# Optimization experiments

Measured on AMD Instinct MI355X. Metric: run time of the kernel, lower is better.

Reference implementation:

```python
import jax, jax.numpy as jnp
import numpy as np
from jax import lax
from jax.scipy.linalg import solve_triangular

SR = 16000
FRAME_PERIOD = 80
FFT_LENGTH = 1024
WIN_MS = 30
EPS = 1e-05
DEFAULT_F0 = 150.0
B, T, N = 8, 320000, 4000

N_BAND = int(np.log2(SR / 600))  # 4
CUTOFF = [SR / 2 ** i for i in range(2, N_BAND + 1)]
CUTOFF.append(CUTOFF[-1])  # [4000, 2000, 1000, 1000]
SEG = [int(c * WIN_MS / 500 + 1.5) for c in CUTOFF]  # [241, 121, 61, 61]

_HHP_VALS = [0.00041447996898231424, 0.0007812505141729248, -0.0010917236836275842,
             -0.001986792567596759, 0.0020903896961562292, 0.004094057027284935,
             -0.0034025808529816698, -0.007496154127205602, 0.004972263339933064,
             0.012738791249119802, -0.006696032689574911, -0.020694051570247052,
             0.008432436565041345, 0.03307438375870053, -0.010018936738799522,
             -0.05423136140580825, 0.011293988915051487, 0.10020081367388213,
             -0.012120546202484579, -0.316300210390957, 0.5124068258062764]
_HLP_VALS = [-0.0006548817007748305, 7.561994958159384e-05, 0.0020408456937895227,
             -0.0007468053532203044, -0.004350223568826493, 0.0025966428382642732,
             0.007639602282756696, -0.006490411890149785, -0.011765804538954506,
             0.013649908479276255, 0.01636866479016021, -0.026075976030529347,
             -0.020910294856659444, 0.04826072503231665, 0.02476784661104811,
             -0.09617846758336064, -0.027359756709866623, 0.3148805216163004,
             0.5282734359405503]

def _qmf_high():
    h = np.zeros(41)
    h[:21] = _HHP_VALS
    h[21:] = h[19::-1]
    return h.astype(np.float32)

def _qmf_low():
    h = np.zeros(37)
    h[:19] = _HLP_VALS
    h[19:] = h[17::-1]
    return h.astype(np.float32)

def _make_window():
    w = np.zeros((N_BAND, SEG[0]), np.float32)
    for i, s in enumerate(SEG):
        w[i, :s] = np.hanning(s + 2)[1:-1]
    return w

def _interp_tables():
    coarse = np.concatenate([[0.0], [SR / 2 ** i for i in range(N_BAND, 0, -1)]])
    freq = np.arange(FFT_LENGTH // 2 + 1) * (SR / FFT_LENGTH)
    idx = np.clip(np.searchsorted(coarse, freq) - 1, 0, len(coarse) - 2)
    x0 = coarse[:-1]
    dx = coarse[1:] - x0
    wts = ((freq - x0[idx]) / dx[idx]).astype(np.float32)
    return idx.astype(np.int32), wts

_HHP = _qmf_high()
_HLP = _qmf_low()
_WIN = _make_window()
_IDX, _WTS = _interp_tables()


def _qmf_conv(x, h):
    # x: (B, T), h: (k,). Reflection pad k//2, cross-correlation, stride 2.
    p = h.shape[0] // 2
    xp = jnp.pad(x, ((0, 0), (p, p)), mode='reflect')
    out = lax.conv_general_dilated(xp[:, None, :], h[None, None, :], (2,), 'VALID',
                                   dimension_numbers=('NCH', 'OIH', 'NCH'))
    return out[:, 0, :]


def setup_inputs() -> dict:
    key = jax.random.key(0)
    k1, k2 = jax.random.split(key)
    x = jax.random.normal(k1, (B, T), jnp.float32)
    f0 = 100.0 + 200.0 * jax.random.uniform(k2, (B, N), jnp.float32)  # 100-300 Hz
    return {"x": x, "f0": f0}


def reference(x, f0):
    hHP = jnp.asarray(_HHP)
    hLP = jnp.asarray(_HLP)
    f0 = lax.stop_gradient(jnp.where(f0 <= 32, DEFAULT_F0, f0))
    Bn, Nf = f0.shape
    time_axis = jnp.arange(Nf, dtype=f0.dtype) * (FRAME_PERIOD / SR)
    bidx = jnp.arange(Bn)[:, None, None]
    eye6 = EPS * jnp.eye(6, dtype=x.dtype)
    lx = x
    bap = []
    for i in range(N_BAND):
        if i < N_BAND - 1:
            hx = _qmf_conv(lx, hHP)
            lx = _qmf_conv(lx, hLP)
            xb = hx
        else:
            xb = lx
        seg = SEG[i]
        tmp_fs = 2.0 * CUTOFF[i]
        pitch = tmp_fs / f0
        t0 = (pitch + 0.5).astype(jnp.int32)
        index_bias = (pitch * 0.5 + 0.5).astype(jnp.int32)
        curr_pos = (time_axis * tmp_fs + 1.5).astype(jnp.int32)[None, :]
        origin = curr_pos - index_bias  # (B, N)
        j = jnp.arange(-1, seg + 1)  # (seg+2,)
        T1 = xb.shape[-1] - 1
        ia = jnp.clip((origin - t0)[..., None] + j, 0, T1)
        ib = jnp.clip((origin + t0)[..., None] + j, 0, T1)
        Ha = xb[bidx, ia]  # (B, N, seg+2)
        Hb = xb[bidx, ib]

        def unfold3(a):  # size-3 sliding windows -> (B, N, seg, 3)
            return jnp.stack([a[..., 0:seg], a[..., 1:seg + 1], a[..., 2:seg + 2]], axis=-1)

        H = jnp.concatenate([unfold3(Ha), unfold3(Hb)], axis=-1)  # (B, N, seg, 6)
        w = jnp.asarray(_WIN[i, :seg])
        Hw = jnp.swapaxes(H, -2, -1) * w  # (B, N, 6, seg)
        R = Hw @ H  # (B, N, 6, 6)
        ig = jnp.clip(origin[..., None] + j[1:-1], 0, T1)
        X = xb[bidx, ig][..., None]  # (B, N, seg, 1)
        L = jnp.linalg.cholesky(R + eye6)
        b = Hw @ X  # (B, N, 6, 1)
        y1 = solve_triangular(L, b, lower=True)
        a = solve_triangular(jnp.swapaxes(L, -2, -1), y1, lower=False)
        HaX = H @ a  # (B, N, seg, 1)
        wsqrt = jnp.sqrt(w)
        wx = wsqrt * X[..., 0]
        wxHa = wsqrt * (X - HaX)[..., 0]
        A = jnp.std(wxHa, axis=-1, ddof=1) / (jnp.std(wx, axis=-1, ddof=1) + 1e-16)
        bap.append(A)
    bap.append(bap[-1])
    ap = jnp.stack(bap[::-1], axis=-1)  # (B, N, n_band+1), low->high freq
    # piecewise-linear interpolation in log domain onto fft bins
    y = jnp.log(ap)
    y0 = y[..., :-1]
    dy = y[..., 1:] - y0
    yi = jnp.take(dy, jnp.asarray(_IDX), axis=-1) * jnp.asarray(_WTS) \
         + jnp.take(y0, jnp.asarray(_IDX), axis=-1)
    return jnp.exp(yi)  # (B, N, fft//2+1)
```

## Files before the change

### kernel.cpp

```cpp
#include <hip/hip_runtime.h>
#include <math.h>

#define NB 8
#define NF 4000
#define NFRAMES (NB * NF)

__constant__ float c_hhp[21] = {
    0.00041447996898231424, 0.0007812505141729248, -0.0010917236836275842,
    -0.001986792567596759,  0.0020903896961562292, 0.004094057027284935,
    -0.0034025808529816698, -0.007496154127205602, 0.004972263339933064,
    0.012738791249119802,   -0.006696032689574911, -0.020694051570247052,
    0.008432436565041345,   0.03307438375870053,   -0.010018936738799522,
    -0.05423136140580825,   0.011293988915051487,  0.10020081367388213,
    -0.012120546202484579,  -0.316300210390957,    0.5124068258062764};
__constant__ float c_hlp[19] = {
    -0.0006548817007748305, 7.561994958159384e-05, 0.0020408456937895227,
    -0.0007468053532203044, -0.004350223568826493, 0.0025966428382642732,
    0.007639602282756696,   -0.006490411890149785, -0.011765804538954506,
    0.013649908479276255,   0.01636866479016021,   -0.026075976030529347,
    -0.020910294856659444,  0.04826072503231665,   0.02476784661104811,
    -0.09617846758336064,   -0.027359756709866623, 0.3148805216163004,
    0.5282734359405503};

__device__ __forceinline__ int reflidx(int i, int len) {
  if (i < 0) i = -i;
  if (i >= len) i = 2 * len - 2 - i;
  return i;
}
__device__ __forceinline__ int clampi(int i, int hi) {
  return min(max(i, 0), hi);
}
__device__ __forceinline__ float4 ld4(const float* p) {
  return *reinterpret_cast<const float4*>(p);
}
__device__ __forceinline__ void st4(float* p, float4 v) {
  *reinterpret_cast<float4*>(p) = v;
}

__global__ __launch_bounds__(256) void qmf_kernel(
    const float* __restrict__ in, int len, float* __restrict__ outH,
    float* __restrict__ outL, float2* __restrict__ wtab) {
  int half = len >> 1;
  int gid = blockIdx.x * 256 + threadIdx.x;
  if (gid >= NB * half) {
    if (wtab) {
      const int segs[4] = {241, 121, 61, 61};
      int k = threadIdx.x;
      for (int i = 0; i < 4; ++i) {
        float v = 0.f;
        if (k < segs[i]) {
          double ang = 2.0 * 3.14159265358979323846 * (double)(k + 1) /
                       (double)(segs[i] + 1);
          v = (float)(0.5 - 0.5 * cos(ang));
        }
        wtab[i * 256 + k] = make_float2(v, sqrtf(v));
      }
    }
    return;
  }
  int b = gid / half;
  int nn = gid - b * half;
  const float* row = in + (size_t)b * len;
  int c = 2 * nn;
  float sh = 0.f, sl = 0.f;
  if (c >= 20 && c <= len - 22) {
    const float2* p2 = reinterpret_cast<const float2*>(row + (c - 20));
    float v[42];
#pragma unroll
    for (int j = 0; j < 21; ++j) {
      float2 t = p2[j];
      v[2 * j] = t.x;
      v[2 * j + 1] = t.y;
    }
#pragma unroll
    for (int t = 0; t < 41; ++t) sh += v[t] * c_hhp[t <= 20 ? t : 40 - t];
#pragma unroll
    for (int t = 0; t < 37; ++t) sl += v[t + 2] * c_hlp[t <= 18 ? t : 36 - t];
  } else {
#pragma unroll
    for (int t = 0; t < 41; ++t)
      sh += row[reflidx(c + t - 20, len)] * c_hhp[t <= 20 ? t : 40 - t];
#pragma unroll
    for (int t = 0; t < 37; ++t)
      sl += row[reflidx(c + t - 18, len)] * c_hlp[t <= 18 ? t : 36 - t];
  }
  outH[(size_t)b * half + nn] = sh;
  outL[(size_t)b * half + nn] = sl;
}

__device__ __forceinline__ void accum1(float wk, float wsk, float h0, float h1,
                                       float h2, float h3, float h4, float h5,
                                       float x, float* __restrict__ rr,
                                       float* __restrict__ bv,
                                       float* __restrict__ gv, float& sxx,
                                       float& s1x) {
  sxx += wk * x * x;
  s1x += wsk * x;
  float wh0 = wk * h0, wh1 = wk * h1, wh2 = wk * h2, wh3 = wk * h3,
        wh4 = wk * h4, wh5 = wk * h5;
  gv[0] += wsk * h0; gv[1] += wsk * h1; gv[2] += wsk * h2;
  gv[3] += wsk * h3; gv[4] += wsk * h4; gv[5] += wsk * h5;
  bv[0] += wh0 * x;  bv[1] += wh1 * x;  bv[2] += wh2 * x;
  bv[3] += wh3 * x;  bv[4] += wh4 * x;  bv[5] += wh5 * x;
  rr[0] += wh0 * h0;  rr[1] += wh0 * h1;  rr[2] += wh0 * h2;
  rr[3] += wh0 * h3;  rr[4] += wh0 * h4;  rr[5] += wh0 * h5;
  rr[6] += wh1 * h1;  rr[7] += wh1 * h2;  rr[8] += wh1 * h3;
  rr[9] += wh1 * h4;  rr[10] += wh1 * h5; rr[11] += wh2 * h2;
  rr[12] += wh2 * h3; rr[13] += wh2 * h4; rr[14] += wh2 * h5;
  rr[15] += wh3 * h3; rr[16] += wh3 * h4; rr[17] += wh3 * h5;
  rr[18] += wh4 * h4; rr[19] += wh4 * h5; rr[20] += wh5 * h5;
}

template <int GS, int NITER, bool CLAMP>
__device__ __forceinline__ void acc_loop(
    const float* __restrict__ row, int T1, int base_a, int base_b, int origin,
    int sub, const float2* __restrict__ wtab, float rr[21], float bv[6],
    float gv[6], float& sxx, float& s1x) {
  if (!CLAMP) {
    const float* pa = row + base_a + 4 * sub;
    const float* pb = row + base_b + 4 * sub;
    const float* pg = row + origin + 4 * sub;
    const float* pw = reinterpret_cast<const float*>(wtab + 4 * sub);
#pragma unroll 2
    for (int j = 0; j < NITER; ++j) {
      const int off = j * 4 * GS;
      float4 a0 = ld4(pa + off);
      float4 a1 = ld4(pa + off + 4);
      float4 b0 = ld4(pb + off);
      float4 b1 = ld4(pb + off + 4);
      float4 xx = ld4(pg + off);
      float4 w01 = ld4(pw + 2 * off);
      float4 w23 = ld4(pw + 2 * off + 4);
      accum1(w01.x, w01.y, a0.x, a0.y, a0.z, b0.x, b0.y, b0.z, xx.x, rr, bv,
             gv, sxx, s1x);
      accum1(w01.z, w01.w, a0.y, a0.z, a0.w, b0.y, b0.z, b0.w, xx.y, rr, bv,
             gv, sxx, s1x);
      accum1(w23.x, w23.y, a0.z, a0.w, a1.x, b0.z, b0.w, b1.x, xx.z, rr, bv,
             gv, sxx, s1x);
      accum1(w23.z, w23.w, a0.w, a1.x, a1.y, b0.w, b1.x, b1.y, xx.w, rr, bv,
             gv, sxx, s1x);
    }
  } else {
#pragma unroll 2
    for (int j = 0; j < NITER; ++j) {
#pragma unroll
      for (int m = 0; m < 4; ++m) {
        int k = 4 * (sub + j * GS) + m;
        float2 wp = wtab[k];
        int ia = base_a + k, ib = base_b + k;
        float h0 = row[clampi(ia, T1)];
        float h1 = row[clampi(ia + 1, T1)];
        float h2 = row[clampi(ia + 2, T1)];
        float h3 = row[clampi(ib, T1)];
        float h4 = row[clampi(ib + 1, T1)];
        float h5 = row[clampi(ib + 2, T1)];
        float x = row[clampi(origin + k, T1)];
        accum1(wp.x, wp.y, h0, h1, h2, h3, h4, h5, x, rr, bv, gv, sxx, s1x);
      }
    }
  }
}

template <int SEG, int LGS, int NITER>
__device__ __forceinline__ void band_body(
    const float* __restrict__ xb, int bandLen, const float* __restrict__ f0,
    float tmp_fs, const float2* __restrict__ wtab, float* __restrict__ Aout,
    int blk) {
  constexpr int GS = 1 << LGS;
  constexpr int FPB = 256 / GS;
  constexpr int KMAX = 4 * GS * NITER;
  const int tid = threadIdx.x;
  const int sub = tid & (GS - 1);
  const int frame = blk * FPB + (tid >> LGS);
  const int b = frame / NF;
  const int n = frame - b * NF;

  float f0v = f0[frame];
  if (f0v <= 32.0f) f0v = 150.0f;
  float pitch = tmp_fs / f0v;
  int t0 = (int)(__fadd_rn(pitch, 0.5f));
  int ibias = (int)(__fadd_rn(__fmul_rn(pitch, 0.5f), 0.5f));
  float tt = __fmul_rn((float)n, 0.005f);
  int curr = (int)(__fadd_rn(__fmul_rn(tt, tmp_fs), 1.5f));
  int origin = curr - ibias;
  const int T1 = bandLen - 1;
  const float* row = xb + (size_t)b * bandLen;
  const int base_a = origin - t0 - 1;
  const int base_b = origin + t0 - 1;

  float rr[21], bv[6], gv[6], sxx = 0.f, s1x = 0.f;
#pragma unroll
  for (int i = 0; i < 21; ++i) rr[i] = 0.f;
#pragma unroll
  for (int i = 0; i < 6; ++i) bv[i] = 0.f;
#pragma unroll
  for (int i = 0; i < 6; ++i) gv[i] = 0.f;

  const bool fast = (base_a >= 0) && (base_b + KMAX + 3 <= T1);
  if (fast)
    acc_loop<GS, NITER, false>(row, T1, base_a, base_b, origin, sub, wtab, rr,
                               bv, gv, sxx, s1x);
  else
    acc_loop<GS, NITER, true>(row, T1, base_a, base_b, origin, sub, wtab, rr,
                              bv, gv, sxx, s1x);

#pragma unroll
  for (int off = GS / 2; off >= 1; off >>= 1) {
#pragma unroll
    for (int i = 0; i < 21; ++i) rr[i] += __shfl_xor(rr[i], off, 64);
#pragma unroll
    for (int i = 0; i < 6; ++i) bv[i] += __shfl_xor(bv[i], off, 64);
    sxx += __shfl_xor(sxx, off, 64);
    s1x += __shfl_xor(s1x, off, 64);
  }

  float M[6][6], invd[6];
  {
    int c = 0;
#pragma unroll
    for (int p = 0; p < 6; ++p)
#pragma unroll
      for (int q = p; q < 6; ++q) {
        M[p][q] = rr[c];
        M[q][p] = rr[c];
        ++c;
      }
#pragma unroll
    for (int p = 0; p < 6; ++p) M[p][p] += 1e-5f;
  }
#pragma unroll
  for (int p = 0; p < 6; ++p) {
    float d = M[p][p];
#pragma unroll
    for (int j = 0; j < 6; ++j)
      if (j < p) d -= M[p][j] * M[p][j];
    d = sqrtf(d);
    M[p][p] = d;
    float inv = 1.0f / d;
    invd[p] = inv;
#pragma unroll
    for (int q = 0; q < 6; ++q)
      if (q > p) {
        float s = M[q][p];
#pragma unroll
        for (int j = 0; j < 6; ++j)
          if (j < p) s -= M[q][j] * M[p][j];
        M[q][p] = s * inv;
      }
  }
  float yv[6], av[6];
#pragma unroll
  for (int p = 0; p < 6; ++p) {
    float s = bv[p];
#pragma unroll
    for (int j = 0; j < 6; ++j)
      if (j < p) s -= M[p][j] * yv[j];
    yv[p] = s * invd[p];
  }
#pragma unroll
  for (int p = 5; p >= 0; --p) {
    float s = yv[p];
#pragma unroll
    for (int j = 0; j < 6; ++j)
      if (j > p) s -= M[j][p] * av[j];
    av[p] = s * invd[p];
  }

  float adotg = av[0] * gv[0] + av[1] * gv[1] + av[2] * gv[2] +
                av[3] * gv[3] + av[4] * gv[4] + av[5] * gv[5];
#pragma unroll
  for (int off = GS / 2; off >= 1; off >>= 1)
    adotg += __shfl_xor(adotg, off, 64);

  float adotb = 0.f, quad = 0.f;
  {
    int c = 0;
#pragma unroll
    for (int p = 0; p < 6; ++p) {
      adotb += av[p] * bv[p];
#pragma unroll
      for (int q = p; q < 6; ++q) {
        float t = av[p] * av[q] * rr[c++];
        quad += (q == p) ? t : 2.f * t;
      }
    }
  }
  if (sub == 0) {
    float s2r = sxx - 2.f * adotb + quad;
    float s1r = s1x - adotg;
    const float nf = (float)SEG;
    float vx = (sxx - s1x * s1x / nf) / (nf - 1.0f);
    float vr = (s2r - s1r * s1r / nf) / (nf - 1.0f);
    float sx = sqrtf(fmaxf(vx, 0.f));
    float sr = sqrtf(fmaxf(vr, 0.f));
    Aout[frame] = sr / (sx + 1e-16f);
  }
}

__global__ __launch_bounds__(256) void bands_kernel(
    const float* __restrict__ hx0, const float* __restrict__ hx1,
    const float* __restrict__ hx2, const float* __restrict__ lx2,
    const float* __restrict__ f0, const float2* __restrict__ wtab,
    float* __restrict__ Aarr) {
  int blk = blockIdx.x;
  if (blk < 1000) {
    band_body<241, 3, 8>(hx0, 160000, f0, 8000.0f, wtab + 0 * 256,
                         Aarr + 0 * NFRAMES, blk);
  } else if (blk < 2000) {
    band_body<121, 3, 4>(hx1, 80000, f0, 4000.0f, wtab + 1 * 256,
                         Aarr + 1 * NFRAMES, blk - 1000);
  } else if (blk < 2500) {
    band_body<61, 2, 4>(hx2, 40000, f0, 2000.0f, wtab + 2 * 256,
                        Aarr + 2 * NFRAMES, blk - 2000);
  } else {
    band_body<61, 2, 4>(lx2, 40000, f0, 2000.0f, wtab + 3 * 256,
                        Aarr + 3 * NFRAMES, blk - 2500);
  }
}

__global__ __launch_bounds__(256) void interp_kernel(
    const float* __restrict__ A, float* __restrict__ out) {
  const int wave = threadIdx.x >> 6;
  const int lane = threadIdx.x & 63;
  const int f = blockIdx.x * 4 + wave;
  float l0 = __logf(A[0 * NFRAMES + f]);
  float l1 = __logf(A[1 * NFRAMES + f]);
  float l2 = __logf(A[2 * NFRAMES + f]);
  float l3 = __logf(A[3 * NFRAMES + f]);
  float d1 = l2 - l3, d2 = l1 - l2, d3 = l0 - l1;
  float* orow = out + (size_t)f * 513;
  float vals[8];
#pragma unroll
  for (int m = 0; m < 8; ++m) {
    int k = 8 * lane + m;
    float y0, dy, c;
    int k0;
    if (k <= 64) {
      y0 = l3; dy = 0.f; k0 = 0; c = 0.015625f;
    } else if (k <= 128) {
      y0 = l3; dy = d1; k0 = 64; c = 0.015625f;
    } else if (k <= 256) {
      y0 = l2; dy = d2; k0 = 128; c = 0.0078125f;
    } else {
      y0 = l1; dy = d3; k0 = 256; c = 0.00390625f;
    }
    float w = (float)(k - k0) * c;
    vals[m] = __expf(y0 + w * dy);
  }
  st4(orow + 8 * lane, make_float4(vals[0], vals[1], vals[2], vals[3]));
  st4(orow + 8 * lane + 4, make_float4(vals[4], vals[5], vals[6], vals[7]));
  if (lane == 0) orow[512] = __expf(l1 + d3);
}

extern "C" void kernel_launch(void* const* d_in, const int* in_sizes, int n_in,
                              void* d_out, int out_size, void* d_ws,
                              size_t ws_size, hipStream_t stream) {
  const float* x = (const float*)d_in[0];
  const float* f0 = (const float*)d_in[1];
  float* out = (float*)d_out;
  float* ws = (float*)d_ws;

  float* hx0 = ws + 0;
  float* lx0 = hx0 + 1280000;
  float* hx1 = lx0 + 1280000;
  float* lx1 = hx1 + 640000;
  float* hx2 = lx1 + 640000;
  float* lx2 = hx2 + 320000;
  float* Aarr = lx2 + 320000;
  float2* wtab = (float2*)(Aarr + 4 * NFRAMES);
  (void)ws_size;

  hipLaunchKernelGGL(qmf_kernel, dim3(5000), dim3(256), 0, stream, x, 320000,
                     hx0, lx0, (float2*)nullptr);
  hipLaunchKernelGGL(qmf_kernel, dim3(2500), dim3(256), 0, stream, lx0,
                     160000, hx1, lx1, (float2*)nullptr);
  hipLaunchKernelGGL(qmf_kernel, dim3(1251), dim3(256), 0, stream, lx1, 80000,
                     hx2, lx2, wtab);

  hipLaunchKernelGGL(bands_kernel, dim3(3000), dim3(256), 0, stream, hx0, hx1,
                     hx2, lx2, f0, wtab, Aarr);

  hipLaunchKernelGGL(interp_kernel, dim3(NFRAMES / 4), dim3(256), 0, stream,
                     Aarr, out);
}
```

Measured before the change: 80.17 us.

## Fuse band regression and log-interpolation into one kernel with per-frame band lanes

Merges the band aperiodicity kernel and the interpolation kernel into one launch: each block handles 8 frames, splitting 32 lanes per frame across the four bands (16/8/4/4), storing log-ratios in LDS and then writing the 513-bin output. This removes a kernel launch and the intermediate A-array round trip through global memory. It adds band-divergent control flow and shuffle reductions within waves, and a block-wide sync before the output write.

```diff
diff --git a/kernel.cpp b/kernel.cpp
--- a/kernel.cpp
+++ b/kernel.cpp
@@ -111,19 +111,66 @@
   rr[18] += wh4 * h4; rr[19] += wh4 * h5; rr[20] += wh5 * h5;
 }
 
-template <int GS, int NITER, bool CLAMP>
-__device__ __forceinline__ void acc_loop(
-    const float* __restrict__ row, int T1, int base_a, int base_b, int origin,
-    int sub, const float2* __restrict__ wtab, float rr[21], float bv[6],
-    float gv[6], float& sxx, float& s1x) {
-  if (!CLAMP) {
+__global__ __launch_bounds__(256) void bands_interp_kernel(
+    const float* __restrict__ hx0, const float* __restrict__ hx1,
+    const float* __restrict__ hx2, const float* __restrict__ lx2,
+    const float* __restrict__ f0, const float2* __restrict__ wtab,
+    float* __restrict__ out) {
+  __shared__ float lds_l[8][4];
+  const int tid = threadIdx.x;
+  const int fslot = tid >> 5;
+  const int lane32 = tid & 31;
+  const int frame = blockIdx.x * 8 + fslot;
+  const int b = frame / NF;
+  const int n = frame - b * NF;
+
+  int band, base, gs;
+  const float* xb;
+  int bandLen;
+  float tmp_fs;
+  if (lane32 < 16) {
+    band = 0; base = 0;  gs = 16; xb = hx0; bandLen = 160000; tmp_fs = 8000.f;
+  } else if (lane32 < 24) {
+    band = 1; base = 16; gs = 8;  xb = hx1; bandLen = 80000;  tmp_fs = 4000.f;
+  } else if (lane32 < 28) {
+    band = 2; base = 24; gs = 4;  xb = hx2; bandLen = 40000;  tmp_fs = 2000.f;
+  } else {
+    band = 3; base = 28; gs = 4;  xb = lx2; bandLen = 40000;  tmp_fs = 2000.f;
+  }
+  const int sub = lane32 - base;
+  const float2* wt = wtab + band * 256;
+
+  float f0v = f0[frame];
+  if (f0v <= 32.0f) f0v = 150.0f;
+  float pitch = tmp_fs / f0v;
+  int t0 = (int)(__fadd_rn(pitch, 0.5f));
+  int ibias = (int)(__fadd_rn(__fmul_rn(pitch, 0.5f), 0.5f));
+  float tt = __fmul_rn((float)n, 0.005f);
+  int curr = (int)(__fadd_rn(__fmul_rn(tt, tmp_fs), 1.5f));
+  int origin = curr - ibias;
+  const int T1 = bandLen - 1;
+  const float* row = xb + (size_t)b * bandLen;
+  const int base_a = origin - t0 - 1;
+  const int base_b = origin + t0 - 1;
+  const int kmax = gs << 4;
+
+  float rr[21], bv[6], gv[6], sxx = 0.f, s1x = 0.f;
+#pragma unroll
+  for (int i = 0; i < 21; ++i) rr[i] = 0.f;
+#pragma unroll
+  for (int i = 0; i < 6; ++i) bv[i] = 0.f;
+#pragma unroll
+  for (int i = 0; i < 6; ++i) gv[i] = 0.f;
+
+  const bool fast = (base_a >= 0) && (base_b + kmax + 3 <= T1);
+  if (fast) {
     const float* pa = row + base_a + 4 * sub;
     const float* pb = row + base_b + 4 * sub;
     const float* pg = row + origin + 4 * sub;
-    const float* pw = reinterpret_cast<const float*>(wtab + 4 * sub);
-#pragma unroll 2
-    for (int j = 0; j < NITER; ++j) {
-      const int off = j * 4 * GS;
+    const float* pw = reinterpret_cast<const float*>(wt + 4 * sub);
+#pragma unroll
+    for (int j = 0; j < 4; ++j) {
+      const int off = j * 4 * gs;
       float4 a0 = ld4(pa + off);
       float4 a1 = ld4(pa + off + 4);
       float4 b0 = ld4(pb + off);
@@ -141,12 +188,12 @@
              gv, sxx, s1x);
     }
   } else {
-#pragma unroll 2
-    for (int j = 0; j < NITER; ++j) {
+#pragma unroll
+    for (int j = 0; j < 4; ++j) {
 #pragma unroll
       for (int m = 0; m < 4; ++m) {
-        int k = 4 * (sub + j * GS) + m;
-        float2 wp = wtab[k];
+        int k = 4 * (sub + j * gs) + m;
+        float2 wp = wt[k];
         int ia = base_a + k, ib = base_b + k;
         float h0 = row[clampi(ia, T1)];
         float h1 = row[clampi(ia + 1, T1)];
@@ -159,60 +206,21 @@
       }
     }
   }
-}
-
-template <int SEG, int LGS, int NITER>
-__device__ __forceinline__ void band_body(
-    const float* __restrict__ xb, int bandLen, const float* __restrict__ f0,
-    float tmp_fs, const float2* __restrict__ wtab, float* __restrict__ Aout,
-    int blk) {
-  constexpr int GS = 1 << LGS;
-  constexpr int FPB = 256 / GS;
-  constexpr int KMAX = 4 * GS * NITER;
-  const int tid = threadIdx.x;
-  const int sub = tid & (GS - 1);
-  const int frame = blk * FPB + (tid >> LGS);
-  const int b = frame / NF;
-  const int n = frame - b * NF;
-
-  float f0v = f0[frame];
-  if (f0v <= 32.0f) f0v = 150.0f;
-  float pitch = tmp_fs / f0v;
-  int t0 = (int)(__fadd_rn(pitch, 0.5f));
-  int ibias = (int)(__fadd_rn(__fmul_rn(pitch, 0.5f), 0.5f));
-  float tt = __fmul_rn((float)n, 0.005f);
-  int curr = (int)(__fadd_rn(__fmul_rn(tt, tmp_fs), 1.5f));
-  int origin = curr - ibias;
-  const int T1 = bandLen - 1;
-  const float* row = xb + (size_t)b * bandLen;
-  const int base_a = origin - t0 - 1;
-  const int base_b = origin + t0 - 1;
-
-  float rr[21], bv[6], gv[6], sxx = 0.f, s1x = 0.f;
-#pragma unroll
-  for (int i = 0; i < 21; ++i) rr[i] = 0.f;
-#pragma unroll
-  for (int i = 0; i < 6; ++i) bv[i] = 0.f;
-#pragma unroll
-  for (int i = 0; i < 6; ++i) gv[i] = 0.f;
-
-  const bool fast = (base_a >= 0) && (base_b + KMAX + 3 <= T1);
-  if (fast)
-    acc_loop<GS, NITER, false>(row, T1, base_a, base_b, origin, sub, wtab, rr,
-                               bv, gv, sxx, s1x);
-  else
-    acc_loop<GS, NITER, true>(row, T1, base_a, base_b, origin, sub, wtab, rr,
-                              bv, gv, sxx, s1x);
-
-#pragma unroll
-  for (int off = GS / 2; off >= 1; off >>= 1) {
-#pragma unroll
-    for (int i = 0; i < 21; ++i) rr[i] += __shfl_xor(rr[i], off, 64);
-#pragma unroll
-    for (int i = 0; i < 6; ++i) bv[i] += __shfl_xor(bv[i], off, 64);
-    sxx += __shfl_xor(sxx, off, 64);
-    s1x += __shfl_xor(s1x, off, 64);
-  }
+
+#define RSTEP(OFF)                                              \
+  do {                                                          \
+    _Pragma("unroll")                                           \
+    for (int i = 0; i < 21; ++i) rr[i] += __shfl_xor(rr[i], OFF, 64); \
+    _Pragma("unroll")                                           \
+    for (int i = 0; i < 6; ++i) bv[i] += __shfl_xor(bv[i], OFF, 64);  \
+    sxx += __shfl_xor(sxx, OFF, 64);                            \
+    s1x += __shfl_xor(s1x, OFF, 64);                            \
+  } while (0)
+  if (band == 0) RSTEP(8);
+  if (band <= 1) RSTEP(4);
+  RSTEP(2);
+  RSTEP(1);
+#undef RSTEP
 
   float M[6][6], invd[6];
   {
@@ -268,9 +276,10 @@
 
   float adotg = av[0] * gv[0] + av[1] * gv[1] + av[2] * gv[2] +
                 av[3] * gv[3] + av[4] * gv[4] + av[5] * gv[5];
-#pragma unroll
-  for (int off = GS / 2; off >= 1; off >>= 1)
-    adotg += __shfl_xor(adotg, off, 64);
+  if (band == 0) adotg += __shfl_xor(adotg, 8, 64);
+  if (band <= 1) adotg += __shfl_xor(adotg, 4, 64);
+  adotg += __shfl_xor(adotg, 2, 64);
+  adotg += __shfl_xor(adotg, 1, 64);
 
   float adotb = 0.f, quad = 0.f;
   {
@@ -288,68 +297,48 @@
   if (sub == 0) {
     float s2r = sxx - 2.f * adotb + quad;
     float s1r = s1x - adotg;
-    const float nf = (float)SEG;
+    const float nf = (band >= 2) ? 61.0f : (band == 1 ? 121.0f : 241.0f);
     float vx = (sxx - s1x * s1x / nf) / (nf - 1.0f);
     float vr = (s2r - s1r * s1r / nf) / (nf - 1.0f);
     float sx = sqrtf(fmaxf(vx, 0.f));
     float sr = sqrtf(fmaxf(vr, 0.f));
-    Aout[frame] = sr / (sx + 1e-16f);
-  }
-}
-
-__global__ __launch_bounds__(256) void bands_kernel(
-    const float* __restrict__ hx0, const float* __restrict__ hx1,
-    const float* __restrict__ hx2, const float* __restrict__ lx2,
-    const float* __restrict__ f0, const float2* __restrict__ wtab,
-    float* __restrict__ Aarr) {
-  int blk = blockIdx.x;
-  if (blk < 1000) {
-    band_body<241, 3, 8>(hx0, 160000, f0, 8000.0f, wtab + 0 * 256,
-                         Aarr + 0 * NFRAMES, blk);
-  } else if (blk < 2000) {
-    band_body<121, 3, 4>(hx1, 80000, f0, 4000.0f, wtab + 1 * 256,
-                         Aarr + 1 * NFRAMES, blk - 1000);
-  } else if (blk < 2500) {
-    band_body<61, 2, 4>(hx2, 40000, f0, 2000.0f, wtab + 2 * 256,
-                        Aarr + 2 * NFRAMES, blk - 2000);
-  } else {
-    band_body<61, 2, 4>(lx2, 40000, f0, 2000.0f, wtab + 3 * 256,
-                        Aarr + 3 * NFRAMES, blk - 2500);
-  }
-}
-
-__global__ __launch_bounds__(256) void interp_kernel(
-    const float* __restrict__ A, float* __restrict__ out) {
-  const int wave = threadIdx.x >> 6;
-  const int lane = threadIdx.x & 63;
-  const int f = blockIdx.x * 4 + wave;
-  float l0 = __logf(A[0 * NFRAMES + f]);
-  float l1 = __logf(A[1 * NFRAMES + f]);
-  float l2 = __logf(A[2 * NFRAMES + f]);
-  float l3 = __logf(A[3 * NFRAMES + f]);
-  float d1 = l2 - l3, d2 = l1 - l2, d3 = l0 - l1;
-  float* orow = out + (size_t)f * 513;
-  float vals[8];
-#pragma unroll
-  for (int m = 0; m < 8; ++m) {
-    int k = 8 * lane + m;
-    float y0, dy, c;
-    int k0;
-    if (k <= 64) {
-      y0 = l3; dy = 0.f; k0 = 0; c = 0.015625f;
-    } else if (k <= 128) {
-      y0 = l3; dy = d1; k0 = 64; c = 0.015625f;
-    } else if (k <= 256) {
-      y0 = l2; dy = d2; k0 = 128; c = 0.0078125f;
-    } else {
-      y0 = l1; dy = d3; k0 = 256; c = 0.00390625f;
-    }
-    float w = (float)(k - k0) * c;
-    vals[m] = __expf(y0 + w * dy);
-  }
-  st4(orow + 8 * lane, make_float4(vals[0], vals[1], vals[2], vals[3]));
-  st4(orow + 8 * lane + 4, make_float4(vals[4], vals[5], vals[6], vals[7]));
-  if (lane == 0) orow[512] = __expf(l1 + d3);
+    lds_l[fslot][band] = __logf(sr / (sx + 1e-16f));
+  }
+  __syncthreads();
+
+  const int w = tid >> 6;
+  const int lane = tid & 63;
+#pragma unroll
+  for (int fr = 0; fr < 2; ++fr) {
+    const int fl = 2 * w + fr;
+    float l0 = lds_l[fl][0];
+    float l1 = lds_l[fl][1];
+    float l2 = lds_l[fl][2];
+    float l3 = lds_l[fl][3];
+    float d1 = l2 - l3, d2 = l1 - l2, d3 = l0 - l1;
+    float* orow = out + (size_t)(blockIdx.x * 8 + fl) * 513;
+    float vals[8];
+#pragma unroll
+    for (int m = 0; m < 8; ++m) {
+      int k = 8 * lane + m;
+      float y0, dy, c;
+      int k0;
+      if (k <= 64) {
+        y0 = l3; dy = 0.f; k0 = 0; c = 0.015625f;
+      } else if (k <= 128) {
+        y0 = l3; dy = d1; k0 = 64; c = 0.015625f;
+      } else if (k <= 256) {
+        y0 = l2; dy = d2; k0 = 128; c = 0.0078125f;
+      } else {
+        y0 = l1; dy = d3; k0 = 256; c = 0.00390625f;
+      }
+      float wq = (float)(k - k0) * c;
+      vals[m] = __expf(y0 + wq * dy);
+    }
+    st4(orow + 8 * lane, make_float4(vals[0], vals[1], vals[2], vals[3]));
+    st4(orow + 8 * lane + 4, make_float4(vals[4], vals[5], vals[6], vals[7]));
+    if (lane == 0) orow[512] = __expf(l1 + d3);
+  }
 }
 
 extern "C" void kernel_launch(void* const* d_in, const int* in_sizes, int n_in,
@@ -366,8 +355,7 @@
   float* lx1 = hx1 + 640000;
   float* hx2 = lx1 + 640000;
   float* lx2 = hx2 + 320000;
-  float* Aarr = lx2 + 320000;
-  float2* wtab = (float2*)(Aarr + 4 * NFRAMES);
+  float2* wtab = (float2*)(lx2 + 320000);
   (void)ws_size;
 
   hipLaunchKernelGGL(qmf_kernel, dim3(5000), dim3(256), 0, stream, x, 320000,
@@ -377,9 +365,6 @@
   hipLaunchKernelGGL(qmf_kernel, dim3(1251), dim3(256), 0, stream, lx1, 80000,
                      hx2, lx2, wtab);
 
-  hipLaunchKernelGGL(bands_kernel, dim3(3000), dim3(256), 0, stream, hx0, hx1,
-                     hx2, lx2, f0, wtab, Aarr);
-
-  hipLaunchKernelGGL(interp_kernel, dim3(NFRAMES / 4), dim3(256), 0, stream,
-                     Aarr, out);
-}
+  hipLaunchKernelGGL(bands_interp_kernel, dim3(NFRAMES / 8), dim3(256), 0,
+                     stream, hx0, hx1, hx2, lx2, f0, wtab, out);
+}
```

Result: slower. 96.43 us (+20.3%).

## Fuse band stages with next QMF level and merge low bands with interpolation

Applied to the files above, without the earlier changes.

Restructures the pipeline so each band's regression runs in the same launch as the next QMF decimation stage. The two lowest bands are fused with the log-domain interpolation, which passes per-frame log values through LDS instead of a separate kernel. This cuts launches from five to four and overlaps independent work within each launch. It also adds a solve_A helper whose result is discarded (dead work the compiler may or may not eliminate), and the last kernel now has only 1000 blocks.

```diff
diff --git a/kernel.cpp b/kernel.cpp
--- a/kernel.cpp
+++ b/kernel.cpp
@@ -37,27 +37,11 @@
   *reinterpret_cast<float4*>(p) = v;
 }
 
-__global__ __launch_bounds__(256) void qmf_kernel(
-    const float* __restrict__ in, int len, float* __restrict__ outH,
-    float* __restrict__ outL, float2* __restrict__ wtab) {
+__device__ __forceinline__ void qmf_body(const float* __restrict__ in, int len,
+                                         float* __restrict__ outH,
+                                         float* __restrict__ outL, int gid) {
   int half = len >> 1;
-  int gid = blockIdx.x * 256 + threadIdx.x;
-  if (gid >= NB * half) {
-    if (wtab) {
-      const int segs[4] = {241, 121, 61, 61};
-      int k = threadIdx.x;
-      for (int i = 0; i < 4; ++i) {
-        float v = 0.f;
-        if (k < segs[i]) {
-          double ang = 2.0 * 3.14159265358979323846 * (double)(k + 1) /
-                       (double)(segs[i] + 1);
-          v = (float)(0.5 - 0.5 * cos(ang));
-        }
-        wtab[i * 256 + k] = make_float2(v, sqrtf(v));
-      }
-    }
-    return;
-  }
+  if (gid >= NB * half) return;
   int b = gid / half;
   int nn = gid - b * half;
   const float* row = in + (size_t)b * len;
@@ -86,6 +70,27 @@
   }
   outH[(size_t)b * half + nn] = sh;
   outL[(size_t)b * half + nn] = sl;
+}
+
+__global__ __launch_bounds__(256) void qmf0_kernel(
+    const float* __restrict__ in, float* __restrict__ outH,
+    float* __restrict__ outL, float2* __restrict__ wtab) {
+  int gid = blockIdx.x * 256 + threadIdx.x;
+  if (gid >= NB * 160000) {
+    const int segs[4] = {241, 121, 61, 61};
+    int k = threadIdx.x;
+    for (int i = 0; i < 4; ++i) {
+      float v = 0.f;
+      if (k < segs[i]) {
+        double ang = 2.0 * 3.14159265358979323846 * (double)(k + 1) /
+                     (double)(segs[i] + 1);
+        v = (float)(0.5 - 0.5 * cos(ang));
+      }
+      wtab[i * 256 + k] = make_float2(v, sqrtf(v));
+    }
+    return;
+  }
+  qmf_body(in, 320000, outH, outL, gid);
 }
 
 __device__ __forceinline__ void accum1(float wk, float wsk, float h0, float h1,
@@ -161,6 +166,82 @@
   }
 }
 
+__device__ __forceinline__ float solve_A(const float rr[21], const float bv[6],
+                                         float adotg_reduced, float sxx,
+                                         float s1x, float nf, float* av) {
+  float M[6][6], invd[6];
+  {
+    int c = 0;
+#pragma unroll
+    for (int p = 0; p < 6; ++p)
+#pragma unroll
+      for (int q = p; q < 6; ++q) {
+        M[p][q] = rr[c];
+        M[q][p] = rr[c];
+        ++c;
+      }
+#pragma unroll
+    for (int p = 0; p < 6; ++p) M[p][p] += 1e-5f;
+  }
+#pragma unroll
+  for (int p = 0; p < 6; ++p) {
+    float d = M[p][p];
+#pragma unroll
+    for (int j = 0; j < 6; ++j)
+      if (j < p) d -= M[p][j] * M[p][j];
+    d = sqrtf(d);
+    M[p][p] = d;
+    float inv = 1.0f / d;
+    invd[p] = inv;
+#pragma unroll
+    for (int q = 0; q < 6; ++q)
+      if (q > p) {
+        float s = M[q][p];
+#pragma unroll
+        for (int j = 0; j < 6; ++j)
+          if (j < p) s -= M[q][j] * M[p][j];
+        M[q][p] = s * inv;
+      }
+  }
+  float yv[6];
+#pragma unroll
+  for (int p = 0; p < 6; ++p) {
+    float s = bv[p];
+#pragma unroll
+    for (int j = 0; j < 6; ++j)
+      if (j < p) s -= M[p][j] * yv[j];
+    yv[p] = s * invd[p];
+  }
+#pragma unroll
+  for (int p = 5; p >= 0; --p) {
+    float s = yv[p];
+#pragma unroll
+    for (int j = 0; j < 6; ++j)
+      if (j > p) s -= M[j][p] * av[j];
+    av[p] = s * invd[p];
+  }
+  float adotb = 0.f, quad = 0.f;
+  {
+    int c = 0;
+#pragma unroll
+    for (int p = 0; p < 6; ++p) {
+      adotb += av[p] * bv[p];
+#pragma unroll
+      for (int q = p; q < 6; ++q) {
+        float t = av[p] * av[q] * rr[c++];
+        quad += (q == p) ? t : 2.f * t;
+      }
+    }
+  }
+  float s2r = sxx - 2.f * adotb + quad;
+  float s1r = s1x - adotg_reduced;
+  float vx = (sxx - s1x * s1x / nf) / (nf - 1.0f);
+  float vr = (s2r - s1r * s1r / nf) / (nf - 1.0f);
+  float sx = sqrtf(fmaxf(vx, 0.f));
+  float sr = sqrtf(fmaxf(vr, 0.f));
+  return sr / (sx + 1e-16f);
+}
+
 template <int SEG, int LGS, int NITER>
 __device__ __forceinline__ void band_body(
     const float* __restrict__ xb, int bandLen, const float* __restrict__ f0,
@@ -214,81 +295,32 @@
     s1x += __shfl_xor(s1x, off, 64);
   }
 
-  float M[6][6], invd[6];
-  {
-    int c = 0;
-#pragma unroll
-    for (int p = 0; p < 6; ++p)
-#pragma unroll
-      for (int q = p; q < 6; ++q) {
-        M[p][q] = rr[c];
-        M[q][p] = rr[c];
-        ++c;
-      }
-#pragma unroll
-    for (int p = 0; p < 6; ++p) M[p][p] += 1e-5f;
-  }
-#pragma unroll
-  for (int p = 0; p < 6; ++p) {
-    float d = M[p][p];
-#pragma unroll
-    for (int j = 0; j < 6; ++j)
-      if (j < p) d -= M[p][j] * M[p][j];
-    d = sqrtf(d);
-    M[p][p] = d;
-    float inv = 1.0f / d;
-    invd[p] = inv;
-#pragma unroll
-    for (int q = 0; q < 6; ++q)
-      if (q > p) {
-        float s = M[q][p];
-#pragma unroll
-        for (int j = 0; j < 6; ++j)
-          if (j < p) s -= M[q][j] * M[p][j];
-        M[q][p] = s * inv;
-      }
-  }
-  float yv[6], av[6];
-#pragma unroll
-  for (int p = 0; p < 6; ++p) {
-    float s = bv[p];
-#pragma unroll
-    for (int j = 0; j < 6; ++j)
-      if (j < p) s -= M[p][j] * yv[j];
-    yv[p] = s * invd[p];
-  }
-#pragma unroll
-  for (int p = 5; p >= 0; --p) {
-    float s = yv[p];
-#pragma unroll
-    for (int j = 0; j < 6; ++j)
-      if (j > p) s -= M[j][p] * av[j];
-    av[p] = s * invd[p];
-  }
-
+  float av[6];
+  float A = solve_A(rr, bv, 0.f, sxx, s1x, (float)SEG, av);
+  (void)A;
   float adotg = av[0] * gv[0] + av[1] * gv[1] + av[2] * gv[2] +
                 av[3] * gv[3] + av[4] * gv[4] + av[5] * gv[5];
 #pragma unroll
   for (int off = GS / 2; off >= 1; off >>= 1)
     adotg += __shfl_xor(adotg, off, 64);
 
-  float adotb = 0.f, quad = 0.f;
-  {
-    int c = 0;
-#pragma unroll
-    for (int p = 0; p < 6; ++p) {
-      adotb += av[p] * bv[p];
-#pragma unroll
-      for (int q = p; q < 6; ++q) {
-        float t = av[p] * av[q] * rr[c++];
-        quad += (q == p) ? t : 2.f * t;
-      }
-    }
-  }
   if (sub == 0) {
+    float adotb = 0.f, quad = 0.f;
+    {
+      int c = 0;
+#pragma unroll
+      for (int p = 0; p < 6; ++p) {
+        adotb += av[p] * bv[p];
+#pragma unroll
+        for (int q = p; q < 6; ++q) {
+          float t = av[p] * av[q] * rr[c++];
+          quad += (q == p) ? t : 2.f * t;
+        }
+      }
+    }
+    const float nf = (float)SEG;
     float s2r = sxx - 2.f * adotb + quad;
     float s1r = s1x - adotg;
-    const float nf = (float)SEG;
     float vx = (sxx - s1x * s1x / nf) / (nf - 1.0f);
     float vr = (s2r - s1r * s1r / nf) / (nf - 1.0f);
     float sx = sqrtf(fmaxf(vx, 0.f));
@@ -297,59 +329,161 @@
   }
 }
 
-__global__ __launch_bounds__(256) void bands_kernel(
-    const float* __restrict__ hx0, const float* __restrict__ hx1,
-    const float* __restrict__ hx2, const float* __restrict__ lx2,
+__global__ __launch_bounds__(256) void band0_qmf1_kernel(
+    const float* __restrict__ lx0, float* __restrict__ hx1,
+    float* __restrict__ lx1, const float* __restrict__ hx0,
     const float* __restrict__ f0, const float2* __restrict__ wtab,
     float* __restrict__ Aarr) {
   int blk = blockIdx.x;
   if (blk < 1000) {
     band_body<241, 3, 8>(hx0, 160000, f0, 8000.0f, wtab + 0 * 256,
                          Aarr + 0 * NFRAMES, blk);
-  } else if (blk < 2000) {
+  } else {
+    qmf_body(lx0, 160000, hx1, lx1, (blk - 1000) * 256 + threadIdx.x);
+  }
+}
+
+__global__ __launch_bounds__(256) void band1_qmf2_kernel(
+    const float* __restrict__ lx1, float* __restrict__ hx2,
+    float* __restrict__ lx2, const float* __restrict__ hx1,
+    const float* __restrict__ f0, const float2* __restrict__ wtab,
+    float* __restrict__ Aarr) {
+  int blk = blockIdx.x;
+  if (blk < 1000) {
     band_body<121, 3, 4>(hx1, 80000, f0, 4000.0f, wtab + 1 * 256,
-                         Aarr + 1 * NFRAMES, blk - 1000);
-  } else if (blk < 2500) {
-    band_body<61, 2, 4>(hx2, 40000, f0, 2000.0f, wtab + 2 * 256,
-                        Aarr + 2 * NFRAMES, blk - 2000);
+                         Aarr + 1 * NFRAMES, blk);
   } else {
-    band_body<61, 2, 4>(lx2, 40000, f0, 2000.0f, wtab + 3 * 256,
-                        Aarr + 3 * NFRAMES, blk - 2500);
-  }
-}
-
-__global__ __launch_bounds__(256) void interp_kernel(
-    const float* __restrict__ A, float* __restrict__ out) {
-  const int wave = threadIdx.x >> 6;
-  const int lane = threadIdx.x & 63;
-  const int f = blockIdx.x * 4 + wave;
-  float l0 = __logf(A[0 * NFRAMES + f]);
-  float l1 = __logf(A[1 * NFRAMES + f]);
-  float l2 = __logf(A[2 * NFRAMES + f]);
-  float l3 = __logf(A[3 * NFRAMES + f]);
-  float d1 = l2 - l3, d2 = l1 - l2, d3 = l0 - l1;
-  float* orow = out + (size_t)f * 513;
-  float vals[8];
-#pragma unroll
-  for (int m = 0; m < 8; ++m) {
-    int k = 8 * lane + m;
-    float y0, dy, c;
-    int k0;
-    if (k <= 64) {
-      y0 = l3; dy = 0.f; k0 = 0; c = 0.015625f;
-    } else if (k <= 128) {
-      y0 = l3; dy = d1; k0 = 64; c = 0.015625f;
-    } else if (k <= 256) {
-      y0 = l2; dy = d2; k0 = 128; c = 0.0078125f;
-    } else {
-      y0 = l1; dy = d3; k0 = 256; c = 0.00390625f;
-    }
-    float w = (float)(k - k0) * c;
-    vals[m] = __expf(y0 + w * dy);
-  }
-  st4(orow + 8 * lane, make_float4(vals[0], vals[1], vals[2], vals[3]));
-  st4(orow + 8 * lane + 4, make_float4(vals[4], vals[5], vals[6], vals[7]));
-  if (lane == 0) orow[512] = __expf(l1 + d3);
+    qmf_body(lx1, 80000, hx2, lx2, (blk - 1000) * 256 + threadIdx.x);
+  }
+}
+
+__global__ __launch_bounds__(256) void bands23_interp_kernel(
+    const float* __restrict__ hx2, const float* __restrict__ lx2,
+    const float* __restrict__ f0, const float2* __restrict__ wtab,
+    const float* __restrict__ Aarr, float* __restrict__ out) {
+  __shared__ float lds_l[32][4];
+  const int tid = threadIdx.x;
+  const int blk = blockIdx.x;
+
+  if (tid < 64) {
+    int f = tid >> 1, band = tid & 1;
+    lds_l[f][band] = __logf(Aarr[band * NFRAMES + blk * 32 + f]);
+  }
+
+  const int half = tid >> 7;
+  const int t7 = tid & 127;
+  const int sub = t7 & 3;
+  const int fslot = t7 >> 2;
+  const int frame = blk * 32 + fslot;
+  const int b = frame / NF;
+  const int n = frame - b * NF;
+  const float* xb = half ? lx2 : hx2;
+  const float2* wt = wtab + (2 + half) * 256;
+
+  float f0v = f0[frame];
+  if (f0v <= 32.0f) f0v = 150.0f;
+  float pitch = 2000.0f / f0v;
+  int t0 = (int)(__fadd_rn(pitch, 0.5f));
+  int ibias = (int)(__fadd_rn(__fmul_rn(pitch, 0.5f), 0.5f));
+  float tt = __fmul_rn((float)n, 0.005f);
+  int curr = (int)(__fadd_rn(__fmul_rn(tt, 2000.0f), 1.5f));
+  int origin = curr - ibias;
+  const int T1 = 40000 - 1;
+  const float* row = xb + (size_t)b * 40000;
+  const int base_a = origin - t0 - 1;
+  const int base_b = origin + t0 - 1;
+
+  float rr[21], bv[6], gv[6], sxx = 0.f, s1x = 0.f;
+#pragma unroll
+  for (int i = 0; i < 21; ++i) rr[i] = 0.f;
+#pragma unroll
+  for (int i = 0; i < 6; ++i) bv[i] = 0.f;
+#pragma unroll
+  for (int i = 0; i < 6; ++i) gv[i] = 0.f;
+
+  const bool fast = (base_a >= 0) && (base_b + 64 + 3 <= T1);
+  if (fast)
+    acc_loop<4, 4, false>(row, T1, base_a, base_b, origin, sub, wt, rr, bv,
+                          gv, sxx, s1x);
+  else
+    acc_loop<4, 4, true>(row, T1, base_a, base_b, origin, sub, wt, rr, bv,
+                         gv, sxx, s1x);
+
+#pragma unroll
+  for (int off = 2; off >= 1; off >>= 1) {
+#pragma unroll
+    for (int i = 0; i < 21; ++i) rr[i] += __shfl_xor(rr[i], off, 64);
+#pragma unroll
+    for (int i = 0; i < 6; ++i) bv[i] += __shfl_xor(bv[i], off, 64);
+    sxx += __shfl_xor(sxx, off, 64);
+    s1x += __shfl_xor(s1x, off, 64);
+  }
+
+  float av[6];
+  float A0 = solve_A(rr, bv, 0.f, sxx, s1x, 61.0f, av);
+  (void)A0;
+  float adotg = av[0] * gv[0] + av[1] * gv[1] + av[2] * gv[2] +
+                av[3] * gv[3] + av[4] * gv[4] + av[5] * gv[5];
+  adotg += __shfl_xor(adotg, 2, 64);
+  adotg += __shfl_xor(adotg, 1, 64);
+
+  if (sub == 0) {
+    float adotb = 0.f, quad = 0.f;
+    {
+      int c = 0;
+#pragma unroll
+      for (int p = 0; p < 6; ++p) {
+        adotb += av[p] * bv[p];
+#pragma unroll
+        for (int q = p; q < 6; ++q) {
+          float t = av[p] * av[q] * rr[c++];
+          quad += (q == p) ? t : 2.f * t;
+        }
+      }
+    }
+    float s2r = sxx - 2.f * adotb + quad;
+    float s1r = s1x - adotg;
+    float vx = (sxx - s1x * s1x / 61.0f) / 60.0f;
+    float vr = (s2r - s1r * s1r / 61.0f) / 60.0f;
+    float sx = sqrtf(fmaxf(vx, 0.f));
+    float sr = sqrtf(fmaxf(vr, 0.f));
+    lds_l[fslot][2 + half] = __logf(sr / (sx + 1e-16f));
+  }
+  __syncthreads();
+
+  const int w = tid >> 6;
+  const int lane = tid & 63;
+#pragma unroll 2
+  for (int p = 0; p < 8; ++p) {
+    const int fl = p * 4 + w;
+    float l0 = lds_l[fl][0];
+    float l1 = lds_l[fl][1];
+    float l2 = lds_l[fl][2];
+    float l3 = lds_l[fl][3];
+    float d1 = l2 - l3, d2 = l1 - l2, d3 = l0 - l1;
+    float* orow = out + (size_t)(blk * 32 + fl) * 513;
+    float vals[8];
+#pragma unroll
+    for (int m = 0; m < 8; ++m) {
+      int k = 8 * lane + m;
+      float y0, dy, c;
+      int k0;
+      if (k <= 64) {
+        y0 = l3; dy = 0.f; k0 = 0; c = 0.015625f;
+      } else if (k <= 128) {
+        y0 = l3; dy = d1; k0 = 64; c = 0.015625f;
+      } else if (k <= 256) {
+        y0 = l2; dy = d2; k0 = 128; c = 0.0078125f;
+      } else {
+        y0 = l1; dy = d3; k0 = 256; c = 0.00390625f;
+      }
+      float wq = (float)(k - k0) * c;
+      vals[m] = __expf(y0 + wq * dy);
+    }
+    st4(orow + 8 * lane, make_float4(vals[0], vals[1], vals[2], vals[3]));
+    st4(orow + 8 * lane + 4, make_float4(vals[4], vals[5], vals[6], vals[7]));
+    if (lane == 0) orow[512] = __expf(l1 + d3);
+  }
 }
 
 extern "C" void kernel_launch(void* const* d_in, const int* in_sizes, int n_in,
@@ -367,19 +501,15 @@
   float* hx2 = lx1 + 640000;
   float* lx2 = hx2 + 320000;
   float* Aarr = lx2 + 320000;
-  float2* wtab = (float2*)(Aarr + 4 * NFRAMES);
+  float2* wtab = (float2*)(Aarr + 2 * NFRAMES);
   (void)ws_size;
 
-  hipLaunchKernelGGL(qmf_kernel, dim3(5000), dim3(256), 0, stream, x, 320000,
-                     hx0, lx0, (float2*)nullptr);
-  hipLaunchKernelGGL(qmf_kernel, dim3(2500), dim3(256), 0, stream, lx0,
-                     160000, hx1, lx1, (float2*)nullptr);
-  hipLaunchKernelGGL(qmf_kernel, dim3(1251), dim3(256), 0, stream, lx1, 80000,
-                     hx2, lx2, wtab);
-
-  hipLaunchKernelGGL(bands_kernel, dim3(3000), dim3(256), 0, stream, hx0, hx1,
-                     hx2, lx2, f0, wtab, Aarr);
-
-  hipLaunchKernelGGL(interp_kernel, dim3(NFRAMES / 4), dim3(256), 0, stream,
-                     Aarr, out);
-}
+  hipLaunchKernelGGL(qmf0_kernel, dim3(5001), dim3(256), 0, stream, x, hx0,
+                     lx0, wtab);
+  hipLaunchKernelGGL(band0_qmf1_kernel, dim3(3500), dim3(256), 0, stream, lx0,
+                     hx1, lx1, hx0, f0, wtab, Aarr);
+  hipLaunchKernelGGL(band1_qmf2_kernel, dim3(2250), dim3(256), 0, stream, lx1,
+                     hx2, lx2, hx1, f0, wtab, Aarr);
+  hipLaunchKernelGGL(bands23_interp_kernel, dim3(1000), dim3(256), 0, stream,
+                     hx2, lx2, f0, wtab, Aarr, out);
+}
```

Result: slower. 83.09 us (+3.7%).
